# Performance work log

Hardware: AMD Instinct MI355X
Metric: run time of the kernel (lower is better)

## Reference

```python
import jax, jax.numpy as jnp
import numpy as np

BS, CAMS, NQ, EMBED = 1, 6, 6400, 256
HEADS, LEVELS, POINTS, DEPTH = 8, 4, 8, 4
DH = EMBED // HEADS
SHAPES = np.array([[64, 176], [32, 88], [16, 44], [8, 22]], dtype=np.int64)  # (H, W) per level
FLEN = int((SHAPES[:, 0] * SHAPES[:, 1]).sum())  # 14960


def setup_inputs() -> dict:
    key = jax.random.key(0)
    ks = jax.random.split(key, 12)
    s = 0.02
    lsi = np.concatenate([[0], np.cumsum(SHAPES[:, 0] * SHAPES[:, 1])[:-1]]).astype(np.int64)
    return {
        'query': jax.random.normal(ks[0], (BS, NQ, EMBED), jnp.float32),
        'key': jax.random.normal(ks[1], (BS, FLEN, CAMS, EMBED), jnp.float32),
        'value': jax.random.normal(ks[2], (BS, FLEN, CAMS, EMBED), jnp.float32),
        'query_pos': jax.random.normal(ks[3], (BS, NQ, EMBED), jnp.float32),
        'reference_points_cam': jax.random.uniform(ks[4], (CAMS, BS, NQ, DEPTH, 2), jnp.float32),
        'bev_mask': jax.random.bernoulli(ks[5], 0.1, (CAMS, BS, NQ, DEPTH)),
        'spatial_shapes': jnp.asarray(SHAPES),
        'level_start_index': jnp.asarray(lsi),
        'Wv': jax.random.normal(ks[6], (EMBED, EMBED), jnp.float32) * s,
        'bv': jnp.zeros((EMBED,), jnp.float32),
        'Wso': jax.random.normal(ks[7], (EMBED, HEADS * LEVELS * POINTS * 2), jnp.float32) * s,
        'bso': jax.random.normal(ks[8], (HEADS * LEVELS * POINTS * 2,), jnp.float32) * s,
        'Waw': jax.random.normal(ks[9], (EMBED, HEADS * LEVELS * POINTS), jnp.float32) * s,
        'baw': jnp.zeros((HEADS * LEVELS * POINTS,), jnp.float32),
        'Wout': jax.random.normal(ks[10], (EMBED, EMBED), jnp.float32) * s,
        'bout': jnp.zeros((EMBED,), jnp.float32),
    }


def _bilinear_gather(v, xi, yi, Wl, Hl):
    # v: (B, Hl*Wl, H, Dh); xi, yi: (B, Nq, H, P) integer-valued floats.
    # grid_sample(padding_mode='zeros'): out-of-range corners contribute 0.
    valid = (xi >= 0) & (xi < Wl) & (yi >= 0) & (yi < Hl)
    idx = (jnp.clip(yi, 0, Hl - 1) * Wl + jnp.clip(xi, 0, Wl - 1)).astype(jnp.int32)
    B, Nq, Hh, P = idx.shape
    idx2 = idx.transpose(0, 1, 3, 2).reshape(B, Nq * P, Hh)[..., None]
    g = jnp.take_along_axis(v, idx2, axis=1)  # (B, Nq*P, Hh, Dh)
    g = g.reshape(B, Nq, P, Hh, -1).transpose(0, 1, 3, 2, 4)  # (B, Nq, Hh, P, Dh)
    return jnp.where(valid[..., None], g, 0.0)


def _msda(v, loc, aw):
    # Multi-scale deformable attn: v (B, Len, H, Dh); loc in [0,1] (B, Nq, H, L, P, 2); aw (B, Nq, H, L, P).
    out = 0.0
    start = 0
    for l in range(LEVELS):
        Hl, Wl = int(SHAPES[l, 0]), int(SHAPES[l, 1])
        vl = v[:, start:start + Hl * Wl]
        start += Hl * Wl
        # align_corners=False pixel coords
        x = loc[:, :, :, l, :, 0] * Wl - 0.5
        y = loc[:, :, :, l, :, 1] * Hl - 0.5
        x0 = jnp.floor(x)
        y0 = jnp.floor(y)
        wx1 = x - x0
        wy1 = y - y0
        s = (_bilinear_gather(vl, x0, y0, Wl, Hl) * ((1 - wx1) * (1 - wy1))[..., None]
             + _bilinear_gather(vl, x0 + 1, y0, Wl, Hl) * (wx1 * (1 - wy1))[..., None]
             + _bilinear_gather(vl, x0, y0 + 1, Wl, Hl) * ((1 - wx1) * wy1)[..., None]
             + _bilinear_gather(vl, x0 + 1, y0 + 1, Wl, Hl) * (wx1 * wy1)[..., None])
        out = out + jnp.einsum('bqhpd,bqhp->bqhd', s, aw[:, :, :, l])
    B, Nq = out.shape[0], out.shape[1]
    return out.reshape(B, Nq, -1)


def reference(query, key, value, query_pos, reference_points_cam, bev_mask,
              spatial_shapes, level_start_index, Wv, bv, Wso, bso, Waw, baw, Wout, bout):
    bs, nq, C = query.shape
    cams = bev_mask.shape[0]
    inp_residual = query  # residual is taken BEFORE query_pos is added
    q = query + query_pos
    # per-camera query visibility from batch-0 mask (as in the torch loop over bev_mask)
    mask_q = jnp.any(bev_mask[:, 0], axis=-1)  # (cams, nq)
    # instead of gather-rebatch to max_len, run attention for all queries and mask the scatter-add
    q_cam = jnp.broadcast_to(q[:, None], (bs, cams, nq, C)).reshape(bs * cams, nq, C)
    ref = jnp.transpose(reference_points_cam, (1, 0, 2, 3, 4)).reshape(bs * cams, nq, DEPTH, 2)
    v = jnp.transpose(value, (2, 0, 1, 3)).reshape(bs * cams, -1, C)
    # MSDeformableAttention3D (BEVFormer): value_proj, offsets, softmax weights, bilinear sampling
    v = (v @ Wv + bv).reshape(bs * cams, -1, HEADS, DH)
    off = (q_cam @ Wso + bso).reshape(bs * cams, nq, HEADS, LEVELS, POINTS, 2)
    norm = jnp.stack([spatial_shapes[:, 1], spatial_shapes[:, 0]], -1).astype(off.dtype)  # (L, 2) = (W, H)
    off = off / norm[None, None, None, :, None, :]
    aw = jax.nn.softmax((q_cam @ Waw + baw).reshape(bs * cams, nq, HEADS, LEVELS * POINTS), axis=-1)
    aw = aw.reshape(bs * cams, nq, HEADS, LEVELS, POINTS)
    pa = POINTS // DEPTH  # xy points per Z anchor
    loc = ref[:, :, None, None, None, :, :] + off.reshape(bs * cams, nq, HEADS, LEVELS, pa, DEPTH, 2)
    loc = loc.reshape(bs * cams, nq, HEADS, LEVELS, POINTS, 2)
    out = _msda(v, loc, aw).reshape(bs, cams, nq, C)
    # scatter-add back: slots[b, q] += sum_cam visible(cam, q) * out[b, cam, q]
    slots = jnp.sum(out * mask_q[None, :, :, None].astype(out.dtype), axis=1)
    count = jnp.any(bev_mask, axis=-1).transpose(1, 2, 0).sum(-1).astype(slots.dtype)  # (bs, nq)
    count = jnp.maximum(count, 1.0)
    slots = slots / count[..., None]
    slots = slots @ Wout + bout
    return slots + inp_residual  # dropout in eval mode = identity
```

## Files before the change

### kernel.cpp

```cpp
#include <hip/hip_runtime.h>
#include <hip/hip_bf16.h>

#define CAMS   6
#define NQ     6400
#define EMBED  256
#define HEADS  8
#define LEVELS 4
#define POINTS 8
#define DEPTH  4
#define DH     32
#define FLEN   14960
#define MV     (FLEN * CAMS)

__constant__ int c_LW[4] = {176, 88, 44, 22};
__constant__ int c_LH[4] = {64, 32, 16, 8};
__constant__ int c_LS[4] = {0, 11264, 14080, 14784};

typedef __bf16 bf16x8 __attribute__((ext_vector_type(8)));
typedef float  f32x4  __attribute__((ext_vector_type(4)));

__device__ __forceinline__ ushort f2bf(float x) {
    __hip_bfloat16 h = __float2bfloat16(x);
    return *(ushort*)&h;
}
__device__ __forceinline__ float bflo(unsigned u) { return __uint_as_float(u << 16); }
__device__ __forceinline__ float bfhi(unsigned u) { return __uint_as_float(u & 0xffff0000u); }

__global__ void detect_mask_fmt(const unsigned* __restrict__ bm, int* __restrict__ flag) {
    int i = blockIdx.x * blockDim.x + threadIdx.x;
    const int total = (CAMS * NQ * DEPTH) / 4;
    unsigned acc = 0;
    for (; i < total; i += gridDim.x * blockDim.x) acc |= bm[i];
    if (acc & 0xFFFFFF00u) atomicOr(flag, 1);
}

__global__ void mask_kernel(const void* __restrict__ bm, const int* __restrict__ flag,
                            int* __restrict__ actmask, float* __restrict__ invcnt) {
    int q = blockIdx.x * blockDim.x + threadIdx.x;
    if (q >= NQ) return;
    int fmt = *flag;
    int cnt = 0, m = 0;
    for (int cam = 0; cam < CAMS; ++cam) {
        int a;
        if (fmt == 1) {
            unsigned w = ((const unsigned*)bm)[cam * NQ + q];
            a = (w != 0u);
        } else {
            int4 v = ((const int4*)bm)[cam * NQ + q];
            a = ((v.x | v.y | v.z | v.w) != 0);
        }
        m |= a << cam;
        cnt += a;
    }
    actmask[q] = m;
    invcnt[q] = 1.0f / (float)(cnt > 0 ? cnt : 1);
}

#define LSTRIDE 40

template <int MODE, int OUT_BF16>
__launch_bounds__(256)
__global__ void gemm_mfma(const float* __restrict__ A,
                          const float* __restrict__ A2,
                          const float* __restrict__ W, int ldw,
                          const float* __restrict__ bias,
                          const float* __restrict__ resid,
                          void* __restrict__ Cout, int ldc, int M) {
    __shared__ ushort sA[128 * LSTRIDE];
    __shared__ ushort sB[128 * LSTRIDE];
    const int t = threadIdx.x;
    const int wave = t >> 6;
    const int lane = t & 63;
    const int wm = wave & 1, wn = wave >> 1;
    const int lane15 = lane & 15;
    const int laneq = lane >> 4;
    const int row0 = blockIdx.x * 128;
    const int col0 = blockIdx.y * 128;

    f32x4 acc[4][4] = {};

    const int a_m = t >> 3;
    const int a_k = (t & 7) * 4;
    const int b_n = t & 127;
    const int b_k = (t >> 7) * 4;

    for (int k0 = 0; k0 < 256; k0 += 32) {
        #pragma unroll
        for (int p = 0; p < 4; ++p) {
            const int m = a_m + p * 32;
            int gm = row0 + m;
            if (gm >= M) gm = M - 1;
            float4 a4 = *(const float4*)(A + (size_t)gm * 256 + k0 + a_k);
            if (MODE == 1) {
                float4 b4 = *(const float4*)(A2 + (size_t)gm * 256 + k0 + a_k);
                a4.x += b4.x; a4.y += b4.y; a4.z += b4.z; a4.w += b4.w;
            } else if (MODE == 2) {
                const float s = A2[gm];
                a4.x *= s; a4.y *= s; a4.z *= s; a4.w *= s;
            }
            ushort4 u = make_ushort4(f2bf(a4.x), f2bf(a4.y), f2bf(a4.z), f2bf(a4.w));
            *(ushort4*)(&sA[m * LSTRIDE + a_k]) = u;
        }
        #pragma unroll
        for (int p = 0; p < 4; ++p) {
            const int k = b_k + p * 8;
            const float* wp = W + (size_t)(k0 + k) * ldw + col0 + b_n;
            const float w0 = wp[0];
            const float w1 = wp[ldw];
            const float w2 = wp[2 * ldw];
            const float w3 = wp[3 * ldw];
            ushort4 u = make_ushort4(f2bf(w0), f2bf(w1), f2bf(w2), f2bf(w3));
            *(ushort4*)(&sB[b_n * LSTRIDE + k]) = u;
        }
        __syncthreads();

        bf16x8 af[4], bfr[4];
        #pragma unroll
        for (int i = 0; i < 4; ++i) {
            const int m = wm * 64 + i * 16 + lane15;
            af[i] = *(const bf16x8*)(&sA[m * LSTRIDE + laneq * 8]);
            const int n = wn * 64 + i * 16 + lane15;
            bfr[i] = *(const bf16x8*)(&sB[n * LSTRIDE + laneq * 8]);
        }
        #pragma unroll
        for (int i = 0; i < 4; ++i)
            #pragma unroll
            for (int j = 0; j < 4; ++j)
                acc[i][j] = __builtin_amdgcn_mfma_f32_16x16x32_bf16(af[i], bfr[j], acc[i][j], 0, 0, 0);
        __syncthreads();
    }

    #pragma unroll
    for (int j = 0; j < 4; ++j) {
        const int col = col0 + wn * 64 + j * 16 + lane15;
        const float bcol = bias[col];
        #pragma unroll
        for (int i = 0; i < 4; ++i) {
            #pragma unroll
            for (int r = 0; r < 4; ++r) {
                const int row = row0 + wm * 64 + i * 16 + laneq * 4 + r;
                if (row < M) {
                    float v = acc[i][j][r] + bcol;
                    if (MODE == 2) v += resid[(size_t)row * 256 + col];
                    if (OUT_BF16)
                        ((ushort*)Cout)[(size_t)row * ldc + col] = f2bf(v);
                    else
                        ((float*)Cout)[(size_t)row * ldc + col] = v;
                }
            }
        }
    }
}

__global__ void softmax_kernel(float* __restrict__ aw) {
    const int t = threadIdx.x;
    const int g = blockIdx.x * 8 + (t >> 5);
    const int j = t & 31;
    float v = aw[g * 32 + j];
    float m = v;
    for (int off = 16; off > 0; off >>= 1) m = fmaxf(m, __shfl_xor(m, off, 32));
    float e = expf(v - m);
    float s = e;
    for (int off = 16; off > 0; off >>= 1) s += __shfl_xor(s, off, 32);
    aw[g * 32 + j] = e / s;
}

__launch_bounds__(256)
__global__ void sample_kernel(const ushort* __restrict__ v,
                              const float* __restrict__ off_ws,
                              const float* __restrict__ aw_ws,
                              const float* __restrict__ rp,
                              const int* __restrict__ actmask,
                              float* __restrict__ slots) {
    const int q = blockIdx.x;
    const int t = threadIdx.x;
    const int h = t >> 5;
    const int e8 = (t >> 2) & 7;
    const int ch8 = (t & 3) * 8;
    const int l = e8 >> 1;
    const int ebase = h * 32 + e8 * 4;

    const int Wl = c_LW[l], Hl = c_LH[l], St = c_LS[l];
    const float fWl = (float)Wl, fHl = (float)Hl;

    float offx[4], offy[4], awv[4];
    #pragma unroll
    for (int j = 0; j < 4; ++j) {
        float2 o = *(const float2*)(off_ws + (size_t)q * 512 + (ebase + j) * 2);
        offx[j] = o.x;
        offy[j] = o.y;
        awv[j] = aw_ws[(size_t)q * 256 + ebase + j];
    }

    const int am = actmask[q];
    float acc[8] = {};

    for (int cam = 0; cam < CAMS; ++cam) {
        if (!((am >> cam) & 1)) continue;

        const float4 r01 = *(const float4*)(rp + (size_t)cam * (NQ * 8) + q * 8);
        const float4 r23 = *(const float4*)(rp + (size_t)cam * (NQ * 8) + q * 8 + 4);
        const float rx[4] = {r01.x, r01.z, r23.x, r23.z};
        const float ry[4] = {r01.y, r01.w, r23.y, r23.w};

        int   addr[16];
        float wgt[16];
        #pragma unroll
        for (int j = 0; j < 4; ++j) {
            const float x = fmaf(rx[j], fWl, offx[j]) - 0.5f;
            const float y = fmaf(ry[j], fHl, offy[j]) - 0.5f;
            const float x0f = floorf(x), y0f = floorf(y);
            const int x0 = (int)x0f, y0 = (int)y0f;
            const float fx = x - x0f, fy = y - y0f;
            const float wx0 = 1.f - fx, wy0 = 1.f - fy;
            #pragma unroll
            for (int c = 0; c < 4; ++c) {
                const int cx = x0 + (c & 1);
                const int cy = y0 + (c >> 1);
                const bool valid = ((unsigned)cx < (unsigned)Wl) & ((unsigned)cy < (unsigned)Hl);
                const int pix = valid ? (St + cy * Wl + cx) : 0;
                addr[j * 4 + c] = (pix * CAMS + cam) * 256 + h * 32 + ch8;
                wgt[j * 4 + c] = valid
                    ? (((c & 1) ? fx : wx0) * ((c >> 1) ? fy : wy0) * awv[j])
                    : 0.f;
            }
        }
        #pragma unroll
        for (int i = 0; i < 16; ++i) {
            const uint4 u = *(const uint4*)(v + addr[i]);
            const float w = wgt[i];
            acc[0] = fmaf(w, bflo(u.x), acc[0]);
            acc[1] = fmaf(w, bfhi(u.x), acc[1]);
            acc[2] = fmaf(w, bflo(u.y), acc[2]);
            acc[3] = fmaf(w, bfhi(u.y), acc[3]);
            acc[4] = fmaf(w, bflo(u.z), acc[4]);
            acc[5] = fmaf(w, bfhi(u.z), acc[5]);
            acc[6] = fmaf(w, bflo(u.w), acc[6]);
            acc[7] = fmaf(w, bfhi(u.w), acc[7]);
        }
    }

    #pragma unroll
    for (int i = 0; i < 8; ++i) {
        acc[i] += __shfl_xor(acc[i], 4);
        acc[i] += __shfl_xor(acc[i], 8);
        acc[i] += __shfl_xor(acc[i], 16);
    }
    slots[(size_t)q * 256 + h * 32 + ch8 + e8] = acc[e8];
}

extern "C" void kernel_launch(void* const* d_in, const int* in_sizes, int n_in,
                              void* d_out, int out_size, void* d_ws, size_t ws_size,
                              hipStream_t stream) {
    const float* query     = (const float*)d_in[0];
    const float* value     = (const float*)d_in[2];
    const float* query_pos = (const float*)d_in[3];
    const float* refpts    = (const float*)d_in[4];
    const void*  bev_mask  = d_in[5];
    const float* Wv   = (const float*)d_in[8];
    const float* bv   = (const float*)d_in[9];
    const float* Wso  = (const float*)d_in[10];
    const float* bso  = (const float*)d_in[11];
    const float* Waw  = (const float*)d_in[12];
    const float* baw  = (const float*)d_in[13];
    const float* Wout = (const float*)d_in[14];
    const float* bout = (const float*)d_in[15];
    float* out = (float*)d_out;

    ushort* v_ws  = (ushort*)d_ws;
    float* off_ws = (float*)(v_ws + (size_t)MV * 256);
    float* aw_ws  = off_ws + (size_t)NQ * 512;
    float* slots  = aw_ws + (size_t)NQ * 256;
    float* invcnt = slots + (size_t)NQ * 256;
    int*   actmask = (int*)(invcnt + NQ);
    int*   flag   = actmask + NQ;

    hipMemsetAsync(flag, 0, sizeof(int), stream);
    hipLaunchKernelGGL(detect_mask_fmt, dim3(64), dim3(256), 0, stream,
                       (const unsigned*)bev_mask, flag);
    hipLaunchKernelGGL(mask_kernel, dim3((NQ + 255) / 256), dim3(256), 0, stream,
                       bev_mask, flag, actmask, invcnt);

    hipLaunchKernelGGL((gemm_mfma<1, 0>), dim3(NQ / 128, 512 / 128), dim3(256), 0, stream,
                       query, query_pos, Wso, 512, bso, nullptr, off_ws, 512, NQ);
    hipLaunchKernelGGL((gemm_mfma<1, 0>), dim3(NQ / 128, 256 / 128), dim3(256), 0, stream,
                       query, query_pos, Waw, 256, baw, nullptr, aw_ws, 256, NQ);
    hipLaunchKernelGGL(softmax_kernel, dim3(NQ * HEADS / 8), dim3(256), 0, stream, aw_ws);

    hipLaunchKernelGGL((gemm_mfma<0, 1>), dim3((MV + 127) / 128, 256 / 128), dim3(256), 0, stream,
                       value, nullptr, Wv, 256, bv, nullptr, v_ws, 256, MV);

    hipLaunchKernelGGL(sample_kernel, dim3(NQ), dim3(256), 0, stream,
                       v_ws, off_ws, aw_ws, refpts, actmask, slots);

    hipLaunchKernelGGL((gemm_mfma<2, 0>), dim3(NQ / 128, 256 / 128), dim3(256), 0, stream,
                       slots, invcnt, Wout, 256, bout, query, out, 256, NQ);
}
```

Measured before the change: 444.4 us.

## Fuse pre-GEMMs, mask and softmax into fewer kernels and relayout value

```diff
diff --git a/kernel.cpp b/kernel.cpp
--- a/kernel.cpp
+++ b/kernel.cpp
@@ -26,56 +26,25 @@
 __device__ __forceinline__ float bflo(unsigned u) { return __uint_as_float(u << 16); }
 __device__ __forceinline__ float bfhi(unsigned u) { return __uint_as_float(u & 0xffff0000u); }
 
-__global__ void detect_mask_fmt(const unsigned* __restrict__ bm, int* __restrict__ flag) {
-    int i = blockIdx.x * blockDim.x + threadIdx.x;
-    const int total = (CAMS * NQ * DEPTH) / 4;
-    unsigned acc = 0;
-    for (; i < total; i += gridDim.x * blockDim.x) acc |= bm[i];
-    if (acc & 0xFFFFFF00u) atomicOr(flag, 1);
-}
-
-__global__ void mask_kernel(const void* __restrict__ bm, const int* __restrict__ flag,
-                            int* __restrict__ actmask, float* __restrict__ invcnt) {
-    int q = blockIdx.x * blockDim.x + threadIdx.x;
-    if (q >= NQ) return;
-    int fmt = *flag;
-    int cnt = 0, m = 0;
-    for (int cam = 0; cam < CAMS; ++cam) {
-        int a;
-        if (fmt == 1) {
-            unsigned w = ((const unsigned*)bm)[cam * NQ + q];
-            a = (w != 0u);
-        } else {
-            int4 v = ((const int4*)bm)[cam * NQ + q];
-            a = ((v.x | v.y | v.z | v.w) != 0);
-        }
-        m |= a << cam;
-        cnt += a;
-    }
-    actmask[q] = m;
-    invcnt[q] = 1.0f / (float)(cnt > 0 ? cnt : 1);
-}
-
 #define LSTRIDE 40
 
-template <int MODE, int OUT_BF16>
-__launch_bounds__(256)
-__global__ void gemm_mfma(const float* __restrict__ A,
-                          const float* __restrict__ A2,
-                          const float* __restrict__ W, int ldw,
-                          const float* __restrict__ bias,
-                          const float* __restrict__ resid,
-                          void* __restrict__ Cout, int ldc, int M) {
-    __shared__ ushort sA[128 * LSTRIDE];
-    __shared__ ushort sB[128 * LSTRIDE];
+template <int MODE, int OUT>
+__device__ __forceinline__ void gemm_body(ushort* sA, ushort* sB,
+                                          const float* __restrict__ A,
+                                          const float* __restrict__ A2,
+                                          const float* __restrict__ W, int ldw,
+                                          const float* __restrict__ bias,
+                                          const float* __restrict__ resid,
+                                          void* __restrict__ Cout, int ldc, int M,
+                                          int bx, int by) {
     const int t = threadIdx.x;
     const int wave = t >> 6;
     const int lane = t & 63;
     const int wm = wave & 1, wn = wave >> 1;
     const int lane15 = lane & 15;
     const int laneq = lane >> 4;
-    const int row0 = blockIdx.x * 128;
-    const int col0 = blockIdx.y * 128;
+    const int row0 = bx * 128;
+    const int col0 = by * 128;
 
     f32x4 acc[4][4] = {};
 
@@ -84,35 +53,57 @@
     const int b_n = t & 127;
     const int b_k = (t >> 7) * 4;
 
+    float4 aR[4], wR[4];
+
+    #pragma unroll
+    for (int p = 0; p < 4; ++p) {
+        int gm = row0 + a_m + p * 32;
+        if (gm >= M) gm = M - 1;
+        aR[p] = *(const float4*)(A + (size_t)gm * 256 + a_k);
+    }
+    #pragma unroll
+    for (int p = 0; p < 4; ++p) {
+        const int k = b_k + p * 8;
+        const float* wp = W + (size_t)k * ldw + col0 + b_n;
+        wR[p] = make_float4(wp[0], wp[ldw], wp[2 * ldw], wp[3 * ldw]);
+    }
+
     for (int k0 = 0; k0 < 256; k0 += 32) {
         #pragma unroll
         for (int p = 0; p < 4; ++p) {
             const int m = a_m + p * 32;
-            int gm = row0 + m;
-            if (gm >= M) gm = M - 1;
-            float4 a4 = *(const float4*)(A + (size_t)gm * 256 + k0 + a_k);
+            float4 a4 = aR[p];
             if (MODE == 1) {
+                int gm = row0 + m;
+                if (gm >= M) gm = M - 1;
                 float4 b4 = *(const float4*)(A2 + (size_t)gm * 256 + k0 + a_k);
                 a4.x += b4.x; a4.y += b4.y; a4.z += b4.z; a4.w += b4.w;
-            } else if (MODE == 2) {
-                const float s = A2[gm];
-                a4.x *= s; a4.y *= s; a4.z *= s; a4.w *= s;
-            }
-            ushort4 u = make_ushort4(f2bf(a4.x), f2bf(a4.y), f2bf(a4.z), f2bf(a4.w));
-            *(ushort4*)(&sA[m * LSTRIDE + a_k]) = u;
+            }
+            *(ushort4*)(&sA[m * LSTRIDE + a_k]) =
+                make_ushort4(f2bf(a4.x), f2bf(a4.y), f2bf(a4.z), f2bf(a4.w));
         }
         #pragma unroll
         for (int p = 0; p < 4; ++p) {
             const int k = b_k + p * 8;
-            const float* wp = W + (size_t)(k0 + k) * ldw + col0 + b_n;
-            const float w0 = wp[0];
-            const float w1 = wp[ldw];
-            const float w2 = wp[2 * ldw];
-            const float w3 = wp[3 * ldw];
-            ushort4 u = make_ushort4(f2bf(w0), f2bf(w1), f2bf(w2), f2bf(w3));
-            *(ushort4*)(&sB[b_n * LSTRIDE + k]) = u;
+            *(ushort4*)(&sB[b_n * LSTRIDE + k]) =
+                make_ushort4(f2bf(wR[p].x), f2bf(wR[p].y), f2bf(wR[p].z), f2bf(wR[p].w));
         }
         __syncthreads();
+
+        if (k0 + 32 < 256) {
+            #pragma unroll
+            for (int p = 0; p < 4; ++p) {
+                int gm = row0 + a_m + p * 32;
+                if (gm >= M) gm = M - 1;
+                aR[p] = *(const float4*)(A + (size_t)gm * 256 + k0 + 32 + a_k);
+            }
+            #pragma unroll
+            for (int p = 0; p < 4; ++p) {
+                const int k = b_k + p * 8;
+                const float* wp = W + (size_t)(k0 + 32 + k) * ldw + col0 + b_n;
+                wR[p] = make_float4(wp[0], wp[ldw], wp[2 * ldw], wp[3 * ldw]);
+            }
+        }
 
         bf16x8 af[4], bfr[4];
         #pragma unroll
@@ -141,36 +132,87 @@
                 const int row = row0 + wm * 64 + i * 16 + laneq * 4 + r;
                 if (row < M) {
                     float v = acc[i][j][r] + bcol;
-                    if (MODE == 2) v += resid[(size_t)row * 256 + col];
-                    if (OUT_BF16)
-                        ((ushort*)Cout)[(size_t)row * ldc + col] = f2bf(v);
-                    else
+                    if (OUT == 1) {
+                        const unsigned pix = ((unsigned)row * 43691u) >> 18;
+                        const unsigned cam = (unsigned)row - pix * 6u;
+                        const int hh = col >> 5, ch = col & 31;
+                        ((ushort*)Cout)[((size_t)(cam * 8 + hh) * FLEN + pix) * 32 + ch] = f2bf(v);
+                    } else {
+                        if (MODE == 3) v += resid[(size_t)row * 256 + col];
                         ((float*)Cout)[(size_t)row * ldc + col] = v;
+                    }
                 }
             }
         }
     }
 }
 
-__global__ void softmax_kernel(float* __restrict__ aw) {
-    const int t = threadIdx.x;
-    const int g = blockIdx.x * 8 + (t >> 5);
-    const int j = t & 31;
-    float v = aw[g * 32 + j];
-    float m = v;
-    for (int off = 16; off > 0; off >>= 1) m = fmaxf(m, __shfl_xor(m, off, 32));
-    float e = expf(v - m);
-    float s = e;
-    for (int off = 16; off > 0; off >>= 1) s += __shfl_xor(s, off, 32);
-    aw[g * 32 + j] = e / s;
+__launch_bounds__(256)
+__global__ void fused_pre_gemm(const float* __restrict__ value,
+                               const float* __restrict__ query,
+                               const float* __restrict__ query_pos,
+                               const float* __restrict__ Wv,  const float* __restrict__ bv,
+                               const float* __restrict__ Wso, const float* __restrict__ bso,
+                               const float* __restrict__ Waw, const float* __restrict__ baw,
+                               const void* __restrict__ bm,
+                               ushort* __restrict__ v_ws,
+                               float* __restrict__ off_ws,
+                               float* __restrict__ aw_ws,
+                               int* __restrict__ flag) {
+    __shared__ ushort sA[128 * LSTRIDE];
+    __shared__ ushort sB[128 * LSTRIDE];
+    const int bid = blockIdx.x;
+    if (bid < 1404) {
+        gemm_body<0, 1>(sA, sB, value, nullptr, Wv, 256, bv, nullptr,
+                        v_ws, 256, MV, bid >> 1, bid & 1);
+    } else if (bid < 1604) {
+        const int r = bid - 1404;
+        gemm_body<1, 0>(sA, sB, query, query_pos, Wso, 512, bso, nullptr,
+                        off_ws, 512, NQ, r >> 2, r & 3);
+    } else if (bid < 1704) {
+        const int r = bid - 1604;
+        gemm_body<1, 0>(sA, sB, query, query_pos, Waw, 256, baw, nullptr,
+                        aw_ws, 256, NQ, r >> 1, r & 1);
+    } else {
+        const int t = threadIdx.x;
+        const uint4* p4 = (const uint4*)bm;
+        unsigned acc = 0;
+        for (int i = t; i < (CAMS * NQ * DEPTH) / 16; i += 256) {
+            const uint4 w = p4[i];
+            acc |= w.x | w.y | w.z | w.w;
+        }
+        #pragma unroll
+        for (int off = 32; off >= 1; off >>= 1) acc |= __shfl_xor(acc, off);
+        unsigned* sred = (unsigned*)sA;
+        if ((t & 63) == 0) sred[t >> 6] = acc;
+        __syncthreads();
+        if (t == 0) {
+            const unsigned a = sred[0] | sred[1] | sred[2] | sred[3];
+            flag[0] = (a & 0xFFFFFF00u) ? 1 : 0;
+        }
+    }
+}
+
+__launch_bounds__(256)
+__global__ void gemm_out_kernel(const float* __restrict__ slots,
+                                const float* __restrict__ Wout,
+                                const float* __restrict__ bout,
+                                const float* __restrict__ query,
+                                float* __restrict__ out) {
+    __shared__ ushort sA[128 * LSTRIDE];
+    __shared__ ushort sB[128 * LSTRIDE];
+    const int bid = blockIdx.x;
+    gemm_body<3, 0>(sA, sB, slots, nullptr, Wout, 256, bout, query,
+                    out, 256, NQ, bid >> 1, bid & 1);
 }
 
 __launch_bounds__(256)
 __global__ void sample_kernel(const ushort* __restrict__ v,
                               const float* __restrict__ off_ws,
-                              const float* __restrict__ aw_ws,
+                              const float* __restrict__ aw_logit,
                               const float* __restrict__ rp,
-                              const int* __restrict__ actmask,
+                              const void* __restrict__ bm,
+                              const int* __restrict__ flag,
                               float* __restrict__ slots) {
     const int q = blockIdx.x;
     const int t = threadIdx.x;
@@ -183,20 +225,53 @@
     const int Wl = c_LW[l], Hl = c_LH[l], St = c_LS[l];
     const float fWl = (float)Wl, fHl = (float)Hl;
 
-    float offx[4], offy[4], awv[4];
-    #pragma unroll
-    for (int j = 0; j < 4; ++j) {
-        float2 o = *(const float2*)(off_ws + (size_t)q * 512 + (ebase + j) * 2);
-        offx[j] = o.x;
-        offy[j] = o.y;
-        awv[j] = aw_ws[(size_t)q * 256 + ebase + j];
-    }
-
-    const int am = actmask[q];
+    const int fmt = *flag;
+    int am = 0, cnt = 0;
+    if (fmt == 1) {
+        #pragma unroll
+        for (int cam = 0; cam < CAMS; ++cam) {
+            const unsigned w = ((const unsigned*)bm)[cam * NQ + q];
+            const int a = (w != 0u);
+            am |= a << cam;
+            cnt += a;
+        }
+    } else {
+        #pragma unroll
+        for (int cam = 0; cam < CAMS; ++cam) {
+            const int4 w = ((const int4*)bm)[cam * NQ + q];
+            const int a = ((w.x | w.y | w.z | w.w) != 0);
+            am |= a << cam;
+            cnt += a;
+        }
+    }
+    const float invq = 1.0f / (float)(cnt > 0 ? cnt : 1);
+
+    const float4 lg = *(const float4*)(aw_logit + (size_t)q * 256 + ebase);
+    float mx = fmaxf(fmaxf(lg.x, lg.y), fmaxf(lg.z, lg.w));
+    mx = fmaxf(mx, __shfl_xor(mx, 4));
+    mx = fmaxf(mx, __shfl_xor(mx, 8));
+    mx = fmaxf(mx, __shfl_xor(mx, 16));
+    const float e0 = expf(lg.x - mx), e1 = expf(lg.y - mx);
+    const float e2 = expf(lg.z - mx), e3 = expf(lg.w - mx);
+    float s = e0 + e1 + e2 + e3;
+    s += __shfl_xor(s, 4);
+    s += __shfl_xor(s, 8);
+    s += __shfl_xor(s, 16);
+    const float sc = invq / s;
+    const float awv[4] = {e0 * sc, e1 * sc, e2 * sc, e3 * sc};
+
+    const float* ofp = off_ws + (size_t)q * 512 + ebase * 2;
+    const float4 o01 = *(const float4*)(ofp);
+    const float4 o23 = *(const float4*)(ofp + 4);
+    const float offx[4] = {o01.x, o01.z, o23.x, o23.z};
+    const float offy[4] = {o01.y, o01.w, o23.y, o23.w};
+
     float acc[8] = {};
 
     for (int cam = 0; cam < CAMS; ++cam) {
         if (!((am >> cam) & 1)) continue;
+
+        const int camhF = (cam * 8 + h) * FLEN + St;
 
         const float4 r01 = *(const float4*)(rp + (size_t)cam * (NQ * 8) + q * 8);
         const float4 r23 = *(const float4*)(rp + (size_t)cam * (NQ * 8) + q * 8 + 4);
@@ -218,8 +293,8 @@
                 const int cx = x0 + (c & 1);
                 const int cy = y0 + (c >> 1);
                 const bool valid = ((unsigned)cx < (unsigned)Wl) & ((unsigned)cy < (unsigned)Hl);
-                const int pix = valid ? (St + cy * Wl + cx) : 0;
-                addr[j * 4 + c] = (pix * CAMS + cam) * 256 + h * 32 + ch8;
+                const int pixo = valid ? (cy * Wl + cx) : 0;
+                addr[j * 4 + c] = ((camhF + pixo) << 5) + ch8;
                 wgt[j * 4 + c] = valid
                     ? (((c & 1) ? fx : wx0) * ((c >> 1) ? fy : wy0) * awv[j])
                     : 0.f;
@@ -271,28 +346,15 @@
     float* off_ws = (float*)(v_ws + (size_t)MV * 256);
     float* aw_ws  = off_ws + (size_t)NQ * 512;
     float* slots  = aw_ws + (size_t)NQ * 256;
-    float* invcnt = slots + (size_t)NQ * 256;
-    int*   actmask = (int*)(invcnt + NQ);
-    int*   flag   = actmask + NQ;
-
-    hipMemsetAsync(flag, 0, sizeof(int), stream);
-    hipLaunchKernelGGL(detect_mask_fmt, dim3(64), dim3(256), 0, stream,
-                       (const unsigned*)bev_mask, flag);
-    hipLaunchKernelGGL(mask_kernel, dim3((NQ + 255) / 256), dim3(256), 0, stream,
-                       bev_mask, flag, actmask, invcnt);
-
-    hipLaunchKernelGGL((gemm_mfma<1, 0>), dim3(NQ / 128, 512 / 128), dim3(256), 0, stream,
-                       query, query_pos, Wso, 512, bso, nullptr, off_ws, 512, NQ);
-    hipLaunchKernelGGL((gemm_mfma<1, 0>), dim3(NQ / 128, 256 / 128), dim3(256), 0, stream,
-                       query, query_pos, Waw, 256, baw, nullptr, aw_ws, 256, NQ);
-    hipLaunchKernelGGL(softmax_kernel, dim3(NQ * HEADS / 8), dim3(256), 0, stream, aw_ws);
-
-    hipLaunchKernelGGL((gemm_mfma<0, 1>), dim3((MV + 127) / 128, 256 / 128), dim3(256), 0, stream,
-                       value, nullptr, Wv, 256, bv, nullptr, v_ws, 256, MV);
+    int*   flag   = (int*)(slots + (size_t)NQ * 256);
+
+    hipLaunchKernelGGL(fused_pre_gemm, dim3(1705), dim3(256), 0, stream,
+                       value, query, query_pos, Wv, bv, Wso, bso, Waw, baw,
+                       bev_mask, v_ws, off_ws, aw_ws, flag);
 
     hipLaunchKernelGGL(sample_kernel, dim3(NQ), dim3(256), 0, stream,
-                       v_ws, off_ws, aw_ws, refpts, actmask, slots);
-
-    hipLaunchKernelGGL((gemm_mfma<2, 0>), dim3(NQ / 128, 256 / 128), dim3(256), 0, stream,
-                       slots, invcnt, Wout, 256, bout, query, out, 256, NQ);
-}
+                       v_ws, off_ws, aw_ws, refpts, bev_mask, flag, slots);
+
+    hipLaunchKernelGGL(gemm_out_kernel, dim3(100), dim3(256), 0, stream,
+                       slots, Wout, bout, query, out);
+}
```

Result: faster. 367.6 us (-17.3%).
